# Kernel optimization log

Hardware: AMD Instinct MI355X
Metric: run time of the kernel (lower is better)

Reference implementation:

```python
import jax, jax.numpy as jnp
import numpy as np

NX = 768
N_HEAD = 12
R = 8
SCALING = 16.0  # lora_alpha*r / r = lora_alpha
NEG = 1e10


def setup_inputs() -> dict:
    key = jax.random.key(0)
    ks = jax.random.split(key, 7)
    B, S = 2, 2048
    return {
        "x": jax.random.normal(ks[0], (B, S, NX), dtype=jnp.float32),
        "w_attn": jax.random.normal(ks[1], (NX, 3 * NX), dtype=jnp.float32) * 0.02,
        "b_attn": jax.random.normal(ks[2], (3 * NX,), dtype=jnp.float32) * 0.02,
        "lora_A": jax.random.normal(ks[3], (3 * R, NX), dtype=jnp.float32) * 0.02,
        "lora_B": jax.random.normal(ks[4], (3 * NX, R), dtype=jnp.float32) * 0.02,
        "w_proj": jax.random.normal(ks[5], (NX, NX), dtype=jnp.float32) * 0.02,
        "b_proj": jax.random.normal(ks[6], (NX,), dtype=jnp.float32) * 0.02,
    }


def reference(x, w_attn, b_attn, lora_A, lora_B, w_proj, b_proj):
    B, S, _ = x.shape
    dh = NX // N_HEAD

    # --- LoRA-augmented QKV projection (MergedLinear, fan_in_fan_out=True, unmerged) ---
    qkv = x @ w_attn + b_attn  # [B,S,3*NX]
    A = lora_A.reshape(3, R, NX)          # per-chunk A_i: [r, nx]
    Bm = lora_B.reshape(3, NX, R)         # per-chunk B_i: [nx, r]
    # x @ (B_i @ A_i).T = (x @ A_i.T) @ B_i.T, grouped over q/k/v chunks c
    t = jnp.einsum('bsd,crd->bscr', x, A)           # [B,S,3,r]
    delta = jnp.einsum('bscr,cer->bsce', t, Bm)     # [B,S,3,nx]
    qkv = qkv + delta.reshape(B, S, 3 * NX) * SCALING

    # --- split heads ---
    q, k, v = jnp.split(qkv, 3, axis=-1)
    q = q.reshape(B, S, N_HEAD, dh).transpose(0, 2, 1, 3)  # [B,H,S,dh]
    k = k.reshape(B, S, N_HEAD, dh).transpose(0, 2, 1, 3)  # [B,H,S,dh]
    v = v.reshape(B, S, N_HEAD, dh).transpose(0, 2, 1, 3)  # [B,H,S,dh]

    # --- manual causal softmax attention (scale=True) ---
    w = jnp.einsum('bhqd,bhkd->bhqk', q, k) / jnp.sqrt(jnp.float32(dh))
    mask = jnp.tril(jnp.ones((S, S), dtype=w.dtype))[None, None]  # tril bias buffer
    w = w * mask - NEG * (1.0 - mask)
    w = jax.nn.softmax(w, axis=-1)
    a = jnp.einsum('bhqk,bhkd->bhqd', w, v)  # [B,H,S,dh]

    # --- merge heads + output projection (Conv1D) ---
    a = a.transpose(0, 2, 1, 3).reshape(B, S, NX)
    a = a @ w_proj + b_proj

    present = jnp.stack([k, v])  # [2,B,H,S,dh]
    return a, present
```

## Files before the change

kernel.cpp:

```cpp
#include <hip/hip_runtime.h>
#include <cstdint>

#define NXC 768
#define NHEAD 12
#define BB 2
#define SS 2048
#define MTOT (BB*SS)
#define NQKV (3*NXC)
#define PRESENT_HALF (BB*NHEAD*SS*64)

typedef __bf16 bf16x8 __attribute__((ext_vector_type(8)));
typedef float f32x4 __attribute__((ext_vector_type(4)));
typedef float f32x16 __attribute__((ext_vector_type(16)));

__device__ __forceinline__ uint16_t f2bf(float f) {
    uint32_t u = __builtin_bit_cast(uint32_t, f);
    uint32_t r = (u + 0x7FFFu + ((u >> 16) & 1u)) >> 16;
    return (uint16_t)r;
}

__device__ __forceinline__ bf16x8 vfrag(ushort4 a, ushort4 b) {
    union { bf16x8 v; ushort4 u[2]; } r;
    r.u[0] = a; r.u[1] = b;
    return r.v;
}

__device__ __forceinline__ void gload16(const uint16_t* g, uint16_t* l) {
    __builtin_amdgcn_global_load_lds(
        (const __attribute__((address_space(1))) unsigned int*)g,
        (__attribute__((address_space(3))) unsigned int*)l, 16, 0, 0);
}


__global__ __launch_bounds__(256) void prep_all(
    const float* __restrict__ x, uint16_t* __restrict__ x_bf,
    const float* __restrict__ w_attn, const float* __restrict__ lora_A,
    const float* __restrict__ lora_B, uint16_t* __restrict__ weffT,
    const float* __restrict__ w_proj, uint16_t* __restrict__ wpT) {
    __shared__ float T[64][65];
    __shared__ float Af[8][64];
    __shared__ float Bf[64][8];
    const int t = threadIdx.x;
    const int blk = blockIdx.x;
    if (blk < 3072) {
        int i = blk * 256 + t;
        float4 v = ((const float4*)x)[i];
        ushort4 o;
        o.x = f2bf(v.x); o.y = f2bf(v.y); o.z = f2bf(v.z); o.w = f2bf(v.w);
        ((ushort4*)x_bf)[i] = o;
        return;
    }
    if (blk < 3504) {
        const int i2 = blk - 3072;
        const int n0 = (i2 % 36) * 64, k0 = (i2 / 36) * 64;
        const int c = n0 / NXC;
        {
            const int nn = t & 63, q = t >> 6;
#pragma unroll
            for (int j = 0; j < 16; ++j) {
                int kr = q + j * 4;
                T[kr][nn] = w_attn[(size_t)(k0 + kr) * NQKV + n0 + nn];
            }
        }
        {
            int idx = t;
            Af[idx >> 6][idx & 63] = lora_A[(size_t)(c * 8 + (idx >> 6)) * NXC + k0 + (idx & 63)];
            idx += 256;
            Af[idx >> 6][idx & 63] = lora_A[(size_t)(c * 8 + (idx >> 6)) * NXC + k0 + (idx & 63)];
            Bf[t >> 3][t & 7] = lora_B[(size_t)(n0 + (t >> 3)) * 8 + (t & 7)];
            idx = t + 256;
            Bf[idx >> 3][idx & 7] = lora_B[(size_t)(n0 + (idx >> 3)) * 8 + (idx & 7)];
        }
        __syncthreads();
        const int kk = t & 63, q = t >> 6;
#pragma unroll
        for (int j = 0; j < 16; ++j) {
            int nn = q + j * 4;
            float d = 0.f;
#pragma unroll
            for (int r = 0; r < 8; ++r) d += Af[r][kk] * Bf[nn][r];
            weffT[(size_t)(n0 + nn) * NXC + k0 + kk] = f2bf(T[kk][nn] + 16.0f * d);
        }
        return;
    }
    {
        const int i3 = blk - 3504;
        const int n0 = (i3 % 12) * 64, k0 = (i3 / 12) * 64;
        {
            const int nn = t & 63, q = t >> 6;
#pragma unroll
            for (int j = 0; j < 16; ++j) {
                int kr = q + j * 4;
                T[kr][nn] = w_proj[(size_t)(k0 + kr) * NXC + n0 + nn];
            }
        }
        __syncthreads();
        const int kk = t & 63, q = t >> 6;
#pragma unroll
        for (int j = 0; j < 16; ++j) {
            int nn = q + j * 4;
            wpT[(size_t)(n0 + nn) * NXC + k0 + kk] = f2bf(T[kk][nn]);
        }
    }
}


template<int MODE, int BM, int BN, int NBX>
__global__ __launch_bounds__(256) void gemm_bt(
    const uint16_t* __restrict__ Abf, const uint16_t* __restrict__ BTbf,
    const float* __restrict__ bias, float* __restrict__ outf,
    uint16_t* __restrict__ q_bf, uint16_t* __restrict__ k_bf,
    uint16_t* __restrict__ vT_bf) {
    constexpr int MR = BM / 32;
    constexpr int NR = BN / 32;
    constexpr int AI = BM / 32;
    constexpr int BI = BN / 32;
    __shared__ uint16_t As[2][BM][64];
    __shared__ uint16_t Bs[2][BN][64];
    const int t = threadIdx.x;
    const int lane = t & 63;
    const int w = t >> 6;
    const int wr = (w >> 1) * (BM / 2);
    const int wc = (w & 1) * (BN / 2);
    const int lr16 = lane & 15;
    const int hi2 = lane >> 4;
    const int id = blockIdx.x;
    const int wgid = (id & 7) * ((int)gridDim.x >> 3) + (id >> 3);
    const int by = wgid / NBX, bx = wgid - by * NBX;
    const size_t arow0 = (size_t)by * BM;
    const size_t brow0 = (size_t)bx * BN;
    const int srow = lane >> 3;
    const int schunk = ((lane & 7) ^ (srow & 7)) << 3;
    const uint16_t* Asrc = Abf + (arow0 + w * (BM / 4) + srow) * NXC + schunk;
    const uint16_t* Bsrc = BTbf + (brow0 + w * (BN / 4) + srow) * NXC + schunk;

    f32x4 acc[MR][NR];
#pragma unroll
    for (int m = 0; m < MR; ++m)
#pragma unroll
        for (int n = 0; n < NR; ++n) acc[m][n] = (f32x4){0.f, 0.f, 0.f, 0.f};

#define STAGE(buf, k0) do { \
    _Pragma("unroll") \
    for (int j = 0; j < AI; ++j) \
        gload16(Asrc + (size_t)(j * 8) * NXC + (k0), &As[buf][w * (BM / 4) + j * 8][0]); \
    _Pragma("unroll") \
    for (int j = 0; j < BI; ++j) \
        gload16(Bsrc + (size_t)(j * 8) * NXC + (k0), &Bs[buf][w * (BN / 4) + j * 8][0]); \
} while (0)

    STAGE(0, 0);
    asm volatile("s_waitcnt vmcnt(0)" ::: "memory");
    __builtin_amdgcn_s_barrier();

    int cur = 0;
    for (int kt = 0; kt < 12; ++kt) {
        if (kt + 1 < 12) STAGE(cur ^ 1, (kt + 1) << 6);
        bf16x8 af[2][MR], bv[2][NR];
#pragma unroll
        for (int kk = 0; kk < 2; ++kk) {
#pragma unroll
            for (int m = 0; m < MR; ++m) {
                const int r = wr + m * 16 + lr16;
                af[kk][m] = *(const bf16x8*)&As[cur][r][(((kk * 4 + hi2) ^ (r & 7)) << 3)];
            }
#pragma unroll
            for (int n = 0; n < NR; ++n) {
                const int r = wc + n * 16 + lr16;
                bv[kk][n] = *(const bf16x8*)&Bs[cur][r][(((kk * 4 + hi2) ^ (r & 7)) << 3)];
            }
        }
        __builtin_amdgcn_s_setprio(1);
#pragma unroll
        for (int kk = 0; kk < 2; ++kk)
#pragma unroll
            for (int m = 0; m < MR; ++m)
#pragma unroll
                for (int n = 0; n < NR; ++n)
                    acc[m][n] = __builtin_amdgcn_mfma_f32_16x16x32_bf16(af[kk][m], bv[kk][n],
                                                                        acc[m][n], 0, 0, 0);
        __builtin_amdgcn_s_setprio(0);
        asm volatile("s_waitcnt vmcnt(0)" ::: "memory");
        __builtin_amdgcn_s_barrier();
        cur ^= 1;
    }
#undef STAGE

    const int rowb = (lane >> 4) << 2;
    const float QSCALE = 0.125f * 1.44269504f;
#pragma unroll
    for (int m = 0; m < MR; ++m) {
        int grow0 = (int)arow0 + wr + m * 16 + rowb;
#pragma unroll
        for (int n = 0; n < NR; ++n) {
            int gcol = (int)brow0 + wc + n * 16 + lr16;
            float bvs = bias[gcol];
            if (MODE == 1) {
#pragma unroll
                for (int ri = 0; ri < 4; ++ri) {
                    int grow = grow0 + ri;
                    outf[(size_t)grow * NXC + gcol] = acc[m][n][ri] + bvs;
                }
            } else {
                int c = gcol >= 2 * NXC ? 2 : (gcol >= NXC ? 1 : 0);
                int e = gcol - c * NXC;
                int h = e >> 6, d = e & 63;
                int b = grow0 >> 11, s0 = grow0 & 2047;
                if (c == 0) {
#pragma unroll
                    for (int ri = 0; ri < 4; ++ri) {
                        float v = acc[m][n][ri] + bvs;
                        q_bf[((size_t)(b * NHEAD + h) * SS + s0 + ri) * 64 + d] = f2bf(v * QSCALE);
                    }
                } else if (c == 1) {
#pragma unroll
                    for (int ri = 0; ri < 4; ++ri) {
                        float v = acc[m][n][ri] + bvs;
                        size_t hidx = (size_t)(b * NHEAD + h) * SS + s0 + ri;
                        k_bf[hidx * 64 + d] = f2bf(v);
                        outf[hidx * 64 + d] = v;
                    }
                } else {
                    float v0 = acc[m][n][0] + bvs, v1 = acc[m][n][1] + bvs;
                    float v2 = acc[m][n][2] + bvs, v3 = acc[m][n][3] + bvs;
                    ushort4 pv;
                    pv.x = f2bf(v0); pv.y = f2bf(v1); pv.z = f2bf(v2); pv.w = f2bf(v3);
                    *(ushort4*)(vT_bf + ((size_t)(b * NHEAD + h) * 64 + d) * SS + s0) = pv;
                    size_t hb = ((size_t)(b * NHEAD + h) * SS + s0) * 64 + d;
                    outf[PRESENT_HALF + hb] = v0;
                    outf[PRESENT_HALF + hb + 64] = v1;
                    outf[PRESENT_HALF + hb + 128] = v2;
                    outf[PRESENT_HALF + hb + 192] = v3;
                }
            }
        }
    }
}


__global__ __launch_bounds__(256) void attn_kernel(
    const uint16_t* __restrict__ qb, const uint16_t* __restrict__ kb,
    const uint16_t* __restrict__ vtb, uint16_t* __restrict__ ab) {
    __shared__ __align__(16) uint8_t smem[49152];
    uint16_t* KT0 = (uint16_t*)smem;
    uint16_t* VT0 = (uint16_t*)(smem + 24576);
    float* Mlp = (float*)smem;
    float* Llp = Mlp + 64;
    float* Ofp = Llp + 64;

    const int t = threadIdx.x;
    const int w = t >> 6, lane = t & 63;
    const int qw = w & 1, khalf = w >> 1;
    const int l31 = lane & 31, hi = lane >> 5;
    const int i8 = lane >> 3, c8 = lane & 7;
    const int id = blockIdx.x;
    const int xcd = id & 7, slot = id >> 3;
    const int lh = slot % 3, qs = slot / 3;
    const int qi = 31 - qs;
    const int bh = xcd * 3 + lh;
    const int qbase = qi * 64;
    const int q = qbase + qw * 32 + l31;
    const uint16_t* qh = qb + (size_t)bh * (SS * 64);
    const uint16_t* kh = kb + (size_t)bh * (SS * 64);
    const uint16_t* vh = vtb + (size_t)bh * (64 * SS);
    const int nkt = qi + 1;

    bf16x8 qf[4];
#pragma unroll
    for (int dc = 0; dc < 4; ++dc)
        qf[dc] = *(const bf16x8*)(qh + (size_t)q * 64 + dc * 16 + hi * 8);

    f32x16 o0, o1;
#pragma unroll
    for (int i = 0; i < 16; ++i) { o0[i] = 0.f; o1[i] = 0.f; }
    float m_run = -1e30f, l_run = 0.f;

    const uint16_t* ksrc = kh + (size_t)i8 * 64 + ((c8 ^ i8) << 3);
    const uint16_t* vsrc = vh + (size_t)i8 * SS + ((c8 ^ i8) << 3);
    const int j0 = (w & 1) * 4;

#define ASTAGE(buf, nb) do { \
    if (khalf == 0) { \
        uint16_t* KTn = KT0 + (buf) * 4096; \
        _Pragma("unroll") \
        for (int j = 0; j < 4; ++j) \
            gload16(ksrc + (size_t)((nb) + (j0 + j) * 8) * 64, KTn + (j0 + j) * 8 * 64); \
    } else { \
        uint16_t* VTn = VT0 + (buf) * 4096; \
        _Pragma("unroll") \
        for (int j = 0; j < 4; ++j) \
            gload16(vsrc + (size_t)((j0 + j) * 8) * SS + (nb), VTn + (j0 + j) * 8 * 64); \
    } \
} while (0)

    ASTAGE(0, 0);
    if (nkt > 1) ASTAGE(1, 64);

    int cur = 0;
    for (int kt = 0; kt < nkt; ++kt) {
        if (kt + 1 < nkt) asm volatile("s_waitcnt vmcnt(4)" ::: "memory");
        else              asm volatile("s_waitcnt vmcnt(0)" ::: "memory");
        __builtin_amdgcn_s_barrier();
        __builtin_amdgcn_sched_barrier(0);
        if (kt + 2 < nkt) {
            int b2 = cur + 2; if (b2 >= 3) b2 -= 3;
            ASTAGE(b2, (kt + 2) << 6);
        }
        const uint16_t* KTc = KT0 + cur * 4096;
        const uint16_t* VTc = VT0 + cur * 4096;

        f32x16 sa;
#pragma unroll
        for (int i = 0; i < 16; ++i) sa[i] = 0.f;
        const int krow = khalf * 32 + l31;
        __builtin_amdgcn_s_setprio(1);
#pragma unroll
        for (int dc = 0; dc < 4; ++dc) {
            bf16x8 kf = *(const bf16x8*)(KTc + krow * 64 + (((dc * 2 + hi) ^ (l31 & 7)) << 3));
            sa = __builtin_amdgcn_mfma_f32_32x32x16_bf16(kf, qf[dc], sa, 0, 0, 0);
        }
        __builtin_amdgcn_s_setprio(0);
        if (kt == qi) {
            const int qrel = qw * 32 + l31;
#pragma unroll
            for (int r = 0; r < 16; ++r) {
                int key = khalf * 32 + (r & 3) + 8 * (r >> 2) + 4 * hi;
                sa[r] = (key > qrel) ? -1e30f : sa[r];
            }
        }
        float m8[8];
#pragma unroll
        for (int g = 0; g < 8; ++g) m8[g] = fmaxf(sa[g * 2], sa[g * 2 + 1]);
        float lm = fmaxf(fmaxf(fmaxf(m8[0], m8[1]), fmaxf(m8[2], m8[3])),
                         fmaxf(fmaxf(m8[4], m8[5]), fmaxf(m8[6], m8[7])));
        if (__any(lm > m_run + 8.f)) {
            float tmf = fmaxf(lm, __shfl_xor(lm, 32));
            float nm = fmaxf(m_run, tmf);
            float corr = __builtin_amdgcn_exp2f(m_run - nm);
            l_run *= corr;
#pragma unroll
            for (int i = 0; i < 16; ++i) { o0[i] *= corr; o1[i] *= corr; }
            m_run = nm;
        }
        float e[16];
#pragma unroll
        for (int r = 0; r < 16; ++r) e[r] = __builtin_amdgcn_exp2f(sa[r] - m_run);
        bf16x8 pa0, pa1;
#pragma unroll
        for (int r = 0; r < 8; ++r) { pa0[r] = (__bf16)e[r]; pa1[r] = (__bf16)e[8 + r]; }
        l_run += ((e[0] + e[1]) + (e[2] + e[3])) + ((e[4] + e[5]) + (e[6] + e[7]))
               + ((e[8] + e[9]) + (e[10] + e[11])) + ((e[12] + e[13]) + (e[14] + e[15]));
        const int rx = l31 & 7;
        __builtin_amdgcn_s_setprio(1);
#pragma unroll
        for (int dblk = 0; dblk < 2; ++dblk) {
            const uint16_t* vrow = VTc + (dblk * 32 + l31) * 64;
            ushort4 v0 = *(const ushort4*)(vrow + (((khalf * 4 + 0) ^ rx) << 3) + hi * 4);
            ushort4 v1 = *(const ushort4*)(vrow + (((khalf * 4 + 1) ^ rx) << 3) + hi * 4);
            ushort4 v2 = *(const ushort4*)(vrow + (((khalf * 4 + 2) ^ rx) << 3) + hi * 4);
            ushort4 v3 = *(const ushort4*)(vrow + (((khalf * 4 + 3) ^ rx) << 3) + hi * 4);
            f32x16 oo = dblk ? o1 : o0;
            oo = __builtin_amdgcn_mfma_f32_32x32x16_bf16(vfrag(v0, v1), pa0, oo, 0, 0, 0);
            oo = __builtin_amdgcn_mfma_f32_32x32x16_bf16(vfrag(v2, v3), pa1, oo, 0, 0, 0);
            if (dblk) o1 = oo; else o0 = oo;
        }
        __builtin_amdgcn_s_setprio(0);
        cur = (cur == 2) ? 0 : cur + 1;
    }
#undef ASTAGE

    __syncthreads();

    const float lf = l_run + __shfl_xor(l_run, 32);
    const int qrow = qw * 32 + l31;
    if (khalf == 1) {
        if (hi == 0) { Mlp[qrow] = m_run; Llp[qrow] = lf; }
#pragma unroll
        for (int dblk = 0; dblk < 2; ++dblk)
#pragma unroll
            for (int rg = 0; rg < 4; ++rg) {
                f32x16 oo = dblk ? o1 : o0;
                f32x4 v;
                v[0] = oo[rg * 4 + 0]; v[1] = oo[rg * 4 + 1];
                v[2] = oo[rg * 4 + 2]; v[3] = oo[rg * 4 + 3];
                *(f32x4*)&Ofp[qrow * 68 + dblk * 32 + rg * 8 + hi * 4] = v;
            }
    }
    __syncthreads();
    if (khalf == 0) {
        const float m2 = Mlp[qrow], l2 = Llp[qrow];
        const float ms = fmaxf(m_run, m2);
        const float wA = __builtin_amdgcn_exp2f(m_run - ms);
        const float wB = __builtin_amdgcn_exp2f(m2 - ms);
        const float inv = 1.f / (lf * wA + l2 * wB);
        const int b = bh / NHEAD, h = bh - b * NHEAD;
        uint16_t* abp = ab + ((size_t)(b * SS + q)) * NXC + h * 64;
#pragma unroll
        for (int dblk = 0; dblk < 2; ++dblk)
#pragma unroll
            for (int rg = 0; rg < 4; ++rg) {
                f32x16 oo = dblk ? o1 : o0;
                f32x4 po = *(const f32x4*)&Ofp[qrow * 68 + dblk * 32 + rg * 8 + hi * 4];
                ushort4 wv;
                wv.x = f2bf((oo[rg * 4 + 0] * wA + po[0] * wB) * inv);
                wv.y = f2bf((oo[rg * 4 + 1] * wA + po[1] * wB) * inv);
                wv.z = f2bf((oo[rg * 4 + 2] * wA + po[2] * wB) * inv);
                wv.w = f2bf((oo[rg * 4 + 3] * wA + po[3] * wB) * inv);
                *(ushort4*)(abp + dblk * 32 + rg * 8 + hi * 4) = wv;
            }
    }
}


extern "C" void kernel_launch(void* const* d_in, const int* in_sizes, int n_in,
                              void* d_out, int out_size, void* d_ws, size_t ws_size,
                              hipStream_t stream) {
    const float* x      = (const float*)d_in[0];
    const float* w_attn = (const float*)d_in[1];
    const float* b_attn = (const float*)d_in[2];
    const float* lora_A = (const float*)d_in[3];
    const float* lora_B = (const float*)d_in[4];
    const float* w_proj = (const float*)d_in[5];
    const float* b_proj = (const float*)d_in[6];
    float* out = (float*)d_out;
    float* present = out + (size_t)MTOT * NXC;

    uint16_t* ws    = (uint16_t*)d_ws;
    uint16_t* x_bf  = ws;
    uint16_t* weffT = x_bf + 3145728;
    uint16_t* wpT   = weffT + 1769472;
    uint16_t* q_bf  = wpT + 589824;
    uint16_t* k_bf  = q_bf + 3145728;
    uint16_t* vT_bf = k_bf + 3145728;
    uint16_t* a_bf  = vT_bf + 3145728;

    prep_all<<<dim3(3648), dim3(256), 0, stream>>>(x, x_bf, w_attn, lora_A, lora_B,
                                                   weffT, w_proj, wpT);
    gemm_bt<0, 128, 64, 36><<<dim3(1152), dim3(256), 0, stream>>>(
        x_bf, weffT, b_attn, present, q_bf, k_bf, vT_bf);
    attn_kernel<<<dim3(768), dim3(256), 0, stream>>>(q_bf, k_bf, vT_bf, a_bf);
    gemm_bt<1, 64, 64, 12><<<dim3(768), dim3(256), 0, stream>>>(
        a_bf, wpT, b_proj, out, nullptr, nullptr, nullptr);
}
```

Baseline: 87.73 us.

## Split attention key range across two blocks and merge partials in a kernel

Each causal query tile's key range is split into two halves processed by separate blocks, doubling the attention grid. Each block writes unnormalized bf16 partial outputs plus running max and sum, and a new merge kernel combines the two halves and normalizes. This targets load imbalance and the low block count from long causal tiles, at the cost of an extra launch, extra global traffic for the partials, and one more bf16 rounding of the unnormalized output.

```diff
diff --git a/kernel.cpp b/kernel.cpp
--- a/kernel.cpp
+++ b/kernel.cpp
@@ -17,6 +17,10 @@
     uint32_t u = __builtin_bit_cast(uint32_t, f);
     uint32_t r = (u + 0x7FFFu + ((u >> 16) & 1u)) >> 16;
     return (uint16_t)r;
+}
+
+__device__ __forceinline__ float bf2f(uint16_t u) {
+    return __builtin_bit_cast(float, (uint32_t)u << 16);
 }
 
 __device__ __forceinline__ bf16x8 vfrag(ushort4 a, ushort4 b) {
@@ -240,7 +244,9 @@
 
 __global__ __launch_bounds__(256) void attn_kernel(
     const uint16_t* __restrict__ qb, const uint16_t* __restrict__ kb,
-    const uint16_t* __restrict__ vtb, uint16_t* __restrict__ ab) {
+    const uint16_t* __restrict__ vtb,
+    float* __restrict__ Mpart, float* __restrict__ Lpart,
+    uint16_t* __restrict__ Opart) {
     __shared__ __align__(16) uint8_t smem[49152];
     uint16_t* KT0 = (uint16_t*)smem;
     uint16_t* VT0 = (uint16_t*)(smem + 24576);
@@ -255,7 +261,9 @@
     const int i8 = lane >> 3, c8 = lane & 7;
     const int id = blockIdx.x;
     const int xcd = id & 7, slot = id >> 3;
-    const int lh = slot % 3, qs = slot / 3;
+    const int lh = slot % 3;
+    const int rem = slot / 3;
+    const int qs = rem >> 1, hf = rem & 1;
     const int qi = 31 - qs;
     const int bh = xcd * 3 + lh;
     const int qbase = qi * 64;
@@ -264,6 +272,9 @@
     const uint16_t* kh = kb + (size_t)bh * (SS * 64);
     const uint16_t* vh = vtb + (size_t)bh * (64 * SS);
     const int nkt = qi + 1;
+    const int nk0 = (nkt + 1) >> 1;
+    const int tb = hf ? nk0 : 0;
+    const int nk = hf ? (nkt - nk0) : nk0;
 
     bf16x8 qf[4];
 #pragma unroll
@@ -293,18 +304,18 @@
     } \
 } while (0)
 
-    ASTAGE(0, 0);
-    if (nkt > 1) ASTAGE(1, 64);
+    if (nk > 0) ASTAGE(0, tb << 6);
+    if (nk > 1) ASTAGE(1, (tb + 1) << 6);
 
     int cur = 0;
-    for (int kt = 0; kt < nkt; ++kt) {
-        if (kt + 1 < nkt) asm volatile("s_waitcnt vmcnt(4)" ::: "memory");
-        else              asm volatile("s_waitcnt vmcnt(0)" ::: "memory");
+    for (int kt = 0; kt < nk; ++kt) {
+        if (kt + 1 < nk) asm volatile("s_waitcnt vmcnt(4)" ::: "memory");
+        else             asm volatile("s_waitcnt vmcnt(0)" ::: "memory");
         __builtin_amdgcn_s_barrier();
         __builtin_amdgcn_sched_barrier(0);
-        if (kt + 2 < nkt) {
+        if (kt + 2 < nk) {
             int b2 = cur + 2; if (b2 >= 3) b2 -= 3;
-            ASTAGE(b2, (kt + 2) << 6);
+            ASTAGE(b2, (tb + kt + 2) << 6);
         }
         const uint16_t* KTc = KT0 + cur * 4096;
         const uint16_t* VTc = VT0 + cur * 4096;
@@ -320,7 +331,7 @@
             sa = __builtin_amdgcn_mfma_f32_32x32x16_bf16(kf, qf[dc], sa, 0, 0, 0);
         }
         __builtin_amdgcn_s_setprio(0);
-        if (kt == qi) {
+        if (tb + kt == qi) {
             const int qrel = qw * 32 + l31;
 #pragma unroll
             for (int r = 0; r < 16; ++r) {
@@ -392,9 +403,13 @@
         const float ms = fmaxf(m_run, m2);
         const float wA = __builtin_amdgcn_exp2f(m_run - ms);
         const float wB = __builtin_amdgcn_exp2f(m2 - ms);
-        const float inv = 1.f / (lf * wA + l2 * wB);
-        const int b = bh / NHEAD, h = bh - b * NHEAD;
-        uint16_t* abp = ab + ((size_t)(b * SS + q)) * NXC + h * 64;
+        const float ltot = lf * wA + l2 * wB;
+        const int pidx = (bh * 32 + qi) * 2 + hf;
+        if (hi == 0) {
+            Mpart[pidx * 64 + qrow] = ms;
+            Lpart[pidx * 64 + qrow] = ltot;
+        }
+        uint16_t* op = Opart + (size_t)pidx * 4096 + qrow * 64;
 #pragma unroll
         for (int dblk = 0; dblk < 2; ++dblk)
 #pragma unroll
@@ -402,12 +417,45 @@
                 f32x16 oo = dblk ? o1 : o0;
                 f32x4 po = *(const f32x4*)&Ofp[qrow * 68 + dblk * 32 + rg * 8 + hi * 4];
                 ushort4 wv;
-                wv.x = f2bf((oo[rg * 4 + 0] * wA + po[0] * wB) * inv);
-                wv.y = f2bf((oo[rg * 4 + 1] * wA + po[1] * wB) * inv);
-                wv.z = f2bf((oo[rg * 4 + 2] * wA + po[2] * wB) * inv);
-                wv.w = f2bf((oo[rg * 4 + 3] * wA + po[3] * wB) * inv);
-                *(ushort4*)(abp + dblk * 32 + rg * 8 + hi * 4) = wv;
-            }
+                wv.x = f2bf(oo[rg * 4 + 0] * wA + po[0] * wB);
+                wv.y = f2bf(oo[rg * 4 + 1] * wA + po[1] * wB);
+                wv.z = f2bf(oo[rg * 4 + 2] * wA + po[2] * wB);
+                wv.w = f2bf(oo[rg * 4 + 3] * wA + po[3] * wB);
+                *(ushort4*)(op + dblk * 32 + rg * 8 + hi * 4) = wv;
+            }
+    }
+}
+
+
+__global__ __launch_bounds__(256) void attn_merge(
+    const float* __restrict__ Mpart, const float* __restrict__ Lpart,
+    const uint16_t* __restrict__ Opart, uint16_t* __restrict__ ab) {
+    const int id = blockIdx.x;
+    const int bh = id >> 5, qi = id & 31;
+    const int t = threadIdx.x;
+    const int row = t >> 2;
+    const int dseg = (t & 3) * 16;
+    const int p0 = id * 2;
+    const float m0 = Mpart[p0 * 64 + row], m1 = Mpart[(p0 + 1) * 64 + row];
+    const float l0 = Lpart[p0 * 64 + row], l1 = Lpart[(p0 + 1) * 64 + row];
+    const float ms = fmaxf(m0, m1);
+    const float w0 = __builtin_amdgcn_exp2f(m0 - ms);
+    const float w1 = __builtin_amdgcn_exp2f(m1 - ms);
+    const float inv = 1.f / (l0 * w0 + l1 * w1);
+    const uint16_t* O0 = Opart + (size_t)p0 * 4096 + row * 64 + dseg;
+    const uint16_t* O1 = Opart + (size_t)(p0 + 1) * 4096 + row * 64 + dseg;
+    const int b = bh / NHEAD, h = bh - b * NHEAD;
+    uint16_t* dst = ab + (size_t)(b * SS + qi * 64 + row) * NXC + h * 64 + dseg;
+#pragma unroll
+    for (int g = 0; g < 4; ++g) {
+        ushort4 a = *(const ushort4*)(O0 + g * 4);
+        ushort4 c = *(const ushort4*)(O1 + g * 4);
+        ushort4 wv;
+        wv.x = f2bf((bf2f(a.x) * w0 + bf2f(c.x) * w1) * inv);
+        wv.y = f2bf((bf2f(a.y) * w0 + bf2f(c.y) * w1) * inv);
+        wv.z = f2bf((bf2f(a.z) * w0 + bf2f(c.z) * w1) * inv);
+        wv.w = f2bf((bf2f(a.w) * w0 + bf2f(c.w) * w1) * inv);
+        *(ushort4*)(dst + g * 4) = wv;
     }
 }
 
@@ -433,12 +481,17 @@
     uint16_t* k_bf  = q_bf + 3145728;
     uint16_t* vT_bf = k_bf + 3145728;
     uint16_t* a_bf  = vT_bf + 3145728;
+    float*    Mpart = (float*)(a_bf + 3145728);
+    float*    Lpart = Mpart + 98304;
+    uint16_t* Opart = (uint16_t*)(Lpart + 98304);
 
     prep_all<<<dim3(3648), dim3(256), 0, stream>>>(x, x_bf, w_attn, lora_A, lora_B,
                                                    weffT, w_proj, wpT);
     gemm_bt<0, 128, 64, 36><<<dim3(1152), dim3(256), 0, stream>>>(
         x_bf, weffT, b_attn, present, q_bf, k_bf, vT_bf);
-    attn_kernel<<<dim3(768), dim3(256), 0, stream>>>(q_bf, k_bf, vT_bf, a_bf);
+    attn_kernel<<<dim3(1536), dim3(256), 0, stream>>>(q_bf, k_bf, vT_bf,
+                                                      Mpart, Lpart, Opart);
+    attn_merge<<<dim3(768), dim3(256), 0, stream>>>(Mpart, Lpart, Opart, a_bf);
     gemm_bt<1, 64, 64, 12><<<dim3(768), dim3(256), 0, stream>>>(
         a_bf, wpT, b_proj, out, nullptr, nullptr, nullptr);
 }
```

New measurement: 90.33 us. 3.0% more time.
